# Performance work log

Measured on AMD Instinct MI355X. Metric: run time of the kernel, lower is better.

Reference implementation:

```python
import jax, jax.numpy as jnp
import numpy as np

B, H, S, D = 2, 8, 4096, 64

def setup_inputs() -> dict:
    key = jax.random.key(0)
    kq, kk, kv = jax.random.split(key, 3)
    queries = jax.random.normal(kq, (B, H, S, D), dtype=jnp.float32)
    keys = jax.random.normal(kk, (B, H, S, D), dtype=jnp.float32)
    values = jax.random.normal(kv, (B, H, S, D), dtype=jnp.float32)
    adj = jnp.zeros((1,), dtype=jnp.int32)  # unused by the module, kept for signature fidelity
    return {"queries": queries, "keys": keys, "values": values, "adj": adj}

def reference(queries, keys, values, adj):
    # scores: [B,H,S,S]; note the original divides by a hard-coded 16, not sqrt(d)
    scores = jnp.einsum('bhqd,bhkd->bhqk', queries, keys) / 16.0
    attn = jax.nn.softmax(scores, axis=-1)
    # dropout p=0.0 -> identity in eval/deterministic mode
    h = jnp.einsum('bhqk,bhkd->bhqd', attn, values)  # [B,H,S,D]
    # original uses .view (a reshape, NOT a transpose) to (S, B, H, D)
    return jnp.reshape(h, (S, B, H, D))
```

## Files before the change

kernel.cpp:

```cpp
#include <hip/hip_runtime.h>
#include <hip/hip_bf16.h>
#include <math.h>

#define S_LEN 4096
#define D_DIM 64
#define NBH   16
#define QPRE  0.09016844f

typedef __attribute__((ext_vector_type(8))) short bf16x8;
typedef __attribute__((ext_vector_type(4))) float f32x4;
typedef __attribute__((ext_vector_type(4))) __fp16 f16x4;
typedef __attribute__((ext_vector_type(2))) __fp16 f16x2;

__device__ __forceinline__ unsigned int pkbf(float lo, float hi) {
  unsigned int ua = __float_as_uint(lo) + 0x8000u;
  unsigned int ub = __float_as_uint(hi) + 0x8000u;
  return __builtin_amdgcn_perm(ub, ua, 0x07060302u);
}
__device__ __forceinline__ unsigned int pkhf(float lo, float hi) {
  f16x2 h = __builtin_amdgcn_cvt_pkrtz(lo, hi);
  return *(unsigned int*)&h;
}

__device__ __forceinline__ void dma16(const unsigned short* g, unsigned short* l) {
  __builtin_amdgcn_global_load_lds(
      (const __attribute__((address_space(1))) unsigned int*)g,
      (__attribute__((address_space(3))) unsigned int*)l, 16, 0, 0);
}

__global__ __launch_bounds__(256) void prep(const float* __restrict__ K,
                                            const float* __restrict__ V,
                                            unsigned short* __restrict__ Kbf,
                                            unsigned short* __restrict__ Vt) {
  const int bh = blockIdx.x >> 6;
  const int kt = blockIdx.x & 63;
  const int tid = threadIdx.x;
  __shared__ unsigned short tile[64][72];

  const float* src = V + ((size_t)bh * S_LEN + kt * 64) * D_DIM;
  float4 vf[4];
#pragma unroll
  for (int p = 0; p < 4; ++p) {
    int i = tid + p * 256;
    vf[p] = *(const float4*)&src[(i >> 4) * D_DIM + (i & 15) * 4];
  }
  const float* ks = K + ((size_t)bh * S_LEN + kt * 64) * D_DIM;
  float4 ka[4];
#pragma unroll
  for (int p = 0; p < 2; ++p) {
    int i = tid + p * 256;
    int row = i >> 3, c = (i & 7) * 8;
    ka[2 * p]     = *(const float4*)&ks[row * D_DIM + c];
    ka[2 * p + 1] = *(const float4*)&ks[row * D_DIM + c + 4];
  }

#pragma unroll
  for (int p = 0; p < 4; ++p) {
    int i = tid + p * 256;
    int row = i >> 4, c = (i & 15) * 4;
    int cs = c ^ (((row >> 4) & 3) << 4);
    unsigned long long w = (unsigned long long)pkhf(vf[p].x, vf[p].y) |
                           ((unsigned long long)pkhf(vf[p].z, vf[p].w) << 32);
    *(unsigned long long*)&tile[row][cs] = w;
  }
  __syncthreads();

  unsigned short* kd = Kbf + ((size_t)bh * S_LEN + kt * 64) * D_DIM;
#pragma unroll
  for (int p = 0; p < 2; ++p) {
    int i = tid + p * 256;
    int row = i >> 3, c = (i & 7) * 8;
    uint4 w;
    w.x = pkbf(ka[2 * p].x, ka[2 * p].y);     w.y = pkbf(ka[2 * p].z, ka[2 * p].w);
    w.z = pkbf(ka[2 * p + 1].x, ka[2 * p + 1].y); w.w = pkbf(ka[2 * p + 1].z, ka[2 * p + 1].w);
    *(uint4*)&kd[row * D_DIM + c] = w;
  }

  const int kc = tid & 7;
#pragma unroll
  for (int p = 0; p < 2; ++p) {
    int d = p * 32 + (tid >> 3);
    int col = d ^ (((kc >> 1) & 3) << 4);
    union { unsigned short u[8]; uint4 v; } t;
#pragma unroll
    for (int i = 0; i < 8; ++i) t.u[i] = tile[kc * 8 + i][col];
    *(uint4*)&Vt[((size_t)bh * D_DIM + d) * S_LEN + kt * 64 + kc * 8] = t.v;
  }
}

__global__ __launch_bounds__(256) void fattn(const float* __restrict__ Q,
                                             const unsigned short* __restrict__ Kbf,
                                             const unsigned short* __restrict__ Vt,
                                             float* __restrict__ O) {
  const int bh   = blockIdx.x >> 5;
  const int qb   = blockIdx.x & 31;
  const int tid  = threadIdx.x;
  const int wave = tid >> 6;
  const int lane = tid & 63;
  const int quad = lane >> 4;
  const int l15  = lane & 15;
  const int rho  = l15 & 7;

  __shared__ unsigned short Ksh[2][64][64];
  __shared__ unsigned short Vsh[3][64][64];

  bf16x8 qf[2][2];
#pragma unroll
  for (int qt = 0; qt < 2; ++qt) {
    const int qg = qb * 128 + wave * 32 + qt * 16 + l15;
    const float* qp = Q + ((size_t)bh * S_LEN + qg) * D_DIM + quad * 8;
#pragma unroll
    for (int h = 0; h < 2; ++h) {
      float4 a = *(const float4*)&qp[h * 32];
      float4 b = *(const float4*)&qp[h * 32 + 4];
      union { unsigned int u[4]; bf16x8 v; } f;
      f.u[0] = pkbf(a.x * QPRE, a.y * QPRE);
      f.u[1] = pkbf(a.z * QPRE, a.w * QPRE);
      f.u[2] = pkbf(b.x * QPRE, b.y * QPRE);
      f.u[3] = pkbf(b.z * QPRE, b.w * QPRE);
      qf[qt][h] = f.v;
    }
  }

  f32x4 ot[2][4];
#pragma unroll
  for (int qt = 0; qt < 2; ++qt)
#pragma unroll
    for (int dt = 0; dt < 4; ++dt) ot[qt][dt] = (f32x4){0.f, 0.f, 0.f, 0.f};
  f32x4 otL[2] = {(f32x4){0.f, 0.f, 0.f, 0.f}, (f32x4){0.f, 0.f, 0.f, 0.f}};
  const f16x4 ones = (f16x4){(__fp16)1.0f, (__fp16)1.0f, (__fp16)1.0f, (__fp16)1.0f};

  const unsigned short* Kb = Kbf + (size_t)bh * S_LEN * D_DIM;
  const unsigned short* Vb = Vt + (size_t)bh * D_DIM * S_LEN;

  const int r_lo = wave * 8 + (lane >> 3);
  const int csrc = ((lane & 7) ^ (lane >> 3)) * 8;

  const int ck0 = (quad ^ rho) * 8;
  const int ck1 = ((quad + 4) ^ rho) * 8;
  const int vrow  = l15 * 128 + (quad & 1) * 8;
  const int rho16 = rho << 4;
  const int vq2   = (quad >> 1) << 4;

#define DMAK(T, B) do { const int t_ = (T); \
  dma16(&Kb[(size_t)(t_ * 64 + r_lo) * 64 + csrc],      &Ksh[B][wave * 8][0]); \
  dma16(&Kb[(size_t)(t_ * 64 + r_lo + 32) * 64 + csrc], &Ksh[B][wave * 8 + 32][0]); } while (0)
#define DMAV(T, B) do { const int t_ = (T); \
  dma16(&Vb[(size_t)r_lo * S_LEN + t_ * 64 + csrc],        &Vsh[B][wave * 8][0]); \
  dma16(&Vb[(size_t)(r_lo + 32) * S_LEN + t_ * 64 + csrc], &Vsh[B][wave * 8 + 32][0]); } while (0)

#define SCORES(KB, PD) do { \
  _Pragma("unroll") \
  for (int mt = 0; mt < 4; ++mt) { \
    const int row_ = mt * 16 + l15; \
    bf16x8 kf0 = *(const bf16x8*)&Ksh[KB][row_][ck0]; \
    bf16x8 kf1 = *(const bf16x8*)&Ksh[KB][row_][ck1]; \
    _Pragma("unroll") \
    for (int qt = 0; qt < 2; ++qt) { \
      f32x4 acc = (f32x4){0.f, 0.f, 0.f, 0.f}; \
      acc = __builtin_amdgcn_mfma_f32_16x16x32_bf16(kf0, qf[qt][0], acc, 0, 0, 0); \
      acc = __builtin_amdgcn_mfma_f32_16x16x32_bf16(kf1, qf[qt][1], acc, 0, 0, 0); \
      PD[mt][qt][0] = pkhf(__builtin_amdgcn_exp2f(acc[0]), __builtin_amdgcn_exp2f(acc[1])); \
      PD[mt][qt][1] = pkhf(__builtin_amdgcn_exp2f(acc[2]), __builtin_amdgcn_exp2f(acc[3])); \
    } \
  } } while (0)

#define PVSTEP(VB, PU) do { \
  const char* vbase = (const char*)&Vsh[VB][0][0]; \
  _Pragma("unroll") \
  for (int mt = 0; mt < 4; ++mt) { \
    const int vb_ = vrow + (((mt << 5) + vq2) ^ rho16); \
    union { unsigned int u[2]; f16x4 v; } pb0, pb1; \
    pb0.u[0] = PU[mt][0][0]; pb0.u[1] = PU[mt][0][1]; \
    pb1.u[0] = PU[mt][1][0]; pb1.u[1] = PU[mt][1][1]; \
    otL[0] = __builtin_amdgcn_mfma_f32_16x16x16f16(ones, pb0.v, otL[0], 0, 0, 0); \
    otL[1] = __builtin_amdgcn_mfma_f32_16x16x16f16(ones, pb1.v, otL[1], 0, 0, 0); \
    _Pragma("unroll") \
    for (int dt = 0; dt < 4; ++dt) { \
      f16x4 va = *(const f16x4*)(vbase + vb_ + dt * 2048); \
      ot[0][dt] = __builtin_amdgcn_mfma_f32_16x16x16f16(va, pb0.v, ot[0][dt], 0, 0, 0); \
      ot[1][dt] = __builtin_amdgcn_mfma_f32_16x16x16f16(va, pb1.v, ot[1][dt], 0, 0, 0); \
    } \
  } } while (0)

#define ITER(KT, KBU, KBL, VBU, VBL, PU, PD) do { \
  __syncthreads(); \
  if ((KT) < 62) { DMAK((KT) + 2, KBL); DMAV((KT) + 2, VBL); } \
  SCORES(KBU, PD); \
  PVSTEP(VBU, PU); } while (0)

  unsigned int pA[4][2][2], pB[4][2][2];

  DMAK(0, 0); DMAV(0, 0);
  __syncthreads();
  SCORES(0, pA);
  DMAK(1, 1); DMAV(1, 1);

  for (int b = 0; b < 60; b += 6) {
    ITER(b + 0, 1, 0, 0, 2, pA, pB);
    ITER(b + 1, 0, 1, 1, 0, pB, pA);
    ITER(b + 2, 1, 0, 2, 1, pA, pB);
    ITER(b + 3, 0, 1, 0, 2, pB, pA);
    ITER(b + 4, 1, 0, 1, 0, pA, pB);
    ITER(b + 5, 0, 1, 2, 1, pB, pA);
  }
  ITER(60, 1, 0, 0, 2, pA, pB);
  ITER(61, 0, 1, 1, 0, pB, pA);
  ITER(62, 1, 0, 2, 1, pA, pB);
  PVSTEP(0, pB);

#pragma unroll
  for (int qt = 0; qt < 2; ++qt) {
    float linv = 1.0f / otL[qt][0];
    const int qg = qb * 128 + wave * 32 + qt * 16 + l15;
    float* orow = O + ((size_t)bh * S_LEN + qg) * D_DIM;
#pragma unroll
    for (int dt = 0; dt < 4; ++dt) {
      float4 w;
      w.x = ot[qt][dt][0] * linv;
      w.y = ot[qt][dt][1] * linv;
      w.z = ot[qt][dt][2] * linv;
      w.w = ot[qt][dt][3] * linv;
      *(float4*)&orow[dt * 16 + quad * 4] = w;
    }
  }
#undef DMAK
#undef DMAV
#undef SCORES
#undef PVSTEP
#undef ITER
}

extern "C" void kernel_launch(void* const* d_in, const int* in_sizes, int n_in,
                              void* d_out, int out_size, void* d_ws, size_t ws_size,
                              hipStream_t stream) {
  const float* Q = (const float*)d_in[0];
  const float* K = (const float*)d_in[1];
  const float* V = (const float*)d_in[2];
  unsigned short* Kbf = (unsigned short*)d_ws;
  unsigned short* Vt  = Kbf + (size_t)NBH * S_LEN * D_DIM;
  float* O = (float*)d_out;

  prep<<<NBH * (S_LEN / 64), 256, 0, stream>>>(K, V, Kbf, Vt);
  fattn<<<NBH * (S_LEN / 128), 256, 0, stream>>>(Q, Kbf, Vt, O);
}
```

Measured before the change: 190.1 us.

## Halve queries per block, compute row sums with VALU, shrink V buffering

Each wave now handles 16 query rows instead of 32, so the grid doubles to 1024 blocks and launch bounds ask for 4 blocks per CU. The row-sum MFMA against a ones vector is replaced by accumulating the exp values in registers and reducing across lanes with shuffles. V buffering drops from triple to double, with V prefetched one tile ahead and K two tiles ahead. Block ordering now interleaves heads so neighbouring blocks read different K/V streams. The aim is more occupancy and fewer MFMAs per element, at the cost of K/V tiles being reused across half as many queries per load, which doubles LDS and L2 traffic per query.

```diff
diff --git a/kernel.cpp b/kernel.cpp
--- a/kernel.cpp
+++ b/kernel.cpp
@@ -71,7 +71,7 @@
     int i = tid + p * 256;
     int row = i >> 3, c = (i & 7) * 8;
     uint4 w;
-    w.x = pkbf(ka[2 * p].x, ka[2 * p].y);     w.y = pkbf(ka[2 * p].z, ka[2 * p].w);
+    w.x = pkbf(ka[2 * p].x, ka[2 * p].y);         w.y = pkbf(ka[2 * p].z, ka[2 * p].w);
     w.z = pkbf(ka[2 * p + 1].x, ka[2 * p + 1].y); w.w = pkbf(ka[2 * p + 1].z, ka[2 * p + 1].w);
     *(uint4*)&kd[row * D_DIM + c] = w;
   }
@@ -88,12 +88,12 @@
   }
 }
 
-__global__ __launch_bounds__(256) void fattn(const float* __restrict__ Q,
-                                             const unsigned short* __restrict__ Kbf,
-                                             const unsigned short* __restrict__ Vt,
-                                             float* __restrict__ O) {
-  const int bh   = blockIdx.x >> 5;
-  const int qb   = blockIdx.x & 31;
+__global__ __launch_bounds__(256, 4) void fattn(const float* __restrict__ Q,
+                                                const unsigned short* __restrict__ Kbf,
+                                                const unsigned short* __restrict__ Vt,
+                                                float* __restrict__ O) {
+  const int bh   = blockIdx.x & 15;
+  const int qb   = blockIdx.x >> 4;
   const int tid  = threadIdx.x;
   const int wave = tid >> 6;
   const int lane = tid & 63;
@@ -102,12 +102,11 @@
   const int rho  = l15 & 7;
 
   __shared__ unsigned short Ksh[2][64][64];
-  __shared__ unsigned short Vsh[3][64][64];
-
-  bf16x8 qf[2][2];
-#pragma unroll
-  for (int qt = 0; qt < 2; ++qt) {
-    const int qg = qb * 128 + wave * 32 + qt * 16 + l15;
+  __shared__ unsigned short Vsh[2][64][64];
+
+  bf16x8 qf[2];
+  {
+    const int qg = qb * 64 + wave * 16 + l15;
     const float* qp = Q + ((size_t)bh * S_LEN + qg) * D_DIM + quad * 8;
 #pragma unroll
     for (int h = 0; h < 2; ++h) {
@@ -118,17 +117,14 @@
       f.u[1] = pkbf(a.z * QPRE, a.w * QPRE);
       f.u[2] = pkbf(b.x * QPRE, b.y * QPRE);
       f.u[3] = pkbf(b.z * QPRE, b.w * QPRE);
-      qf[qt][h] = f.v;
+      qf[h] = f.v;
     }
   }
 
-  f32x4 ot[2][4];
-#pragma unroll
-  for (int qt = 0; qt < 2; ++qt)
-#pragma unroll
-    for (int dt = 0; dt < 4; ++dt) ot[qt][dt] = (f32x4){0.f, 0.f, 0.f, 0.f};
-  f32x4 otL[2] = {(f32x4){0.f, 0.f, 0.f, 0.f}, (f32x4){0.f, 0.f, 0.f, 0.f}};
-  const f16x4 ones = (f16x4){(__fp16)1.0f, (__fp16)1.0f, (__fp16)1.0f, (__fp16)1.0f};
+  f32x4 ot[4];
+#pragma unroll
+  for (int dt = 0; dt < 4; ++dt) ot[dt] = (f32x4){0.f, 0.f, 0.f, 0.f};
+  float Lp = 0.f;
 
   const unsigned short* Kb = Kbf + (size_t)bh * S_LEN * D_DIM;
   const unsigned short* Vb = Vt + (size_t)bh * D_DIM * S_LEN;
@@ -155,14 +151,16 @@
     const int row_ = mt * 16 + l15; \
     bf16x8 kf0 = *(const bf16x8*)&Ksh[KB][row_][ck0]; \
     bf16x8 kf1 = *(const bf16x8*)&Ksh[KB][row_][ck1]; \
-    _Pragma("unroll") \
-    for (int qt = 0; qt < 2; ++qt) { \
-      f32x4 acc = (f32x4){0.f, 0.f, 0.f, 0.f}; \
-      acc = __builtin_amdgcn_mfma_f32_16x16x32_bf16(kf0, qf[qt][0], acc, 0, 0, 0); \
-      acc = __builtin_amdgcn_mfma_f32_16x16x32_bf16(kf1, qf[qt][1], acc, 0, 0, 0); \
-      PD[mt][qt][0] = pkhf(__builtin_amdgcn_exp2f(acc[0]), __builtin_amdgcn_exp2f(acc[1])); \
-      PD[mt][qt][1] = pkhf(__builtin_amdgcn_exp2f(acc[2]), __builtin_amdgcn_exp2f(acc[3])); \
-    } \
+    f32x4 acc = (f32x4){0.f, 0.f, 0.f, 0.f}; \
+    acc = __builtin_amdgcn_mfma_f32_16x16x32_bf16(kf0, qf[0], acc, 0, 0, 0); \
+    acc = __builtin_amdgcn_mfma_f32_16x16x32_bf16(kf1, qf[1], acc, 0, 0, 0); \
+    float p0 = __builtin_amdgcn_exp2f(acc[0]); \
+    float p1 = __builtin_amdgcn_exp2f(acc[1]); \
+    float p2 = __builtin_amdgcn_exp2f(acc[2]); \
+    float p3 = __builtin_amdgcn_exp2f(acc[3]); \
+    Lp += (p0 + p1) + (p2 + p3); \
+    PD[mt][0] = pkhf(p0, p1); \
+    PD[mt][1] = pkhf(p2, p3); \
   } } while (0)
 
 #define PVSTEP(VB, PU) do { \
@@ -170,59 +168,51 @@
   _Pragma("unroll") \
   for (int mt = 0; mt < 4; ++mt) { \
     const int vb_ = vrow + (((mt << 5) + vq2) ^ rho16); \
-    union { unsigned int u[2]; f16x4 v; } pb0, pb1; \
-    pb0.u[0] = PU[mt][0][0]; pb0.u[1] = PU[mt][0][1]; \
-    pb1.u[0] = PU[mt][1][0]; pb1.u[1] = PU[mt][1][1]; \
-    otL[0] = __builtin_amdgcn_mfma_f32_16x16x16f16(ones, pb0.v, otL[0], 0, 0, 0); \
-    otL[1] = __builtin_amdgcn_mfma_f32_16x16x16f16(ones, pb1.v, otL[1], 0, 0, 0); \
+    union { unsigned int u[2]; f16x4 v; } pb; \
+    pb.u[0] = PU[mt][0]; pb.u[1] = PU[mt][1]; \
     _Pragma("unroll") \
     for (int dt = 0; dt < 4; ++dt) { \
       f16x4 va = *(const f16x4*)(vbase + vb_ + dt * 2048); \
-      ot[0][dt] = __builtin_amdgcn_mfma_f32_16x16x16f16(va, pb0.v, ot[0][dt], 0, 0, 0); \
-      ot[1][dt] = __builtin_amdgcn_mfma_f32_16x16x16f16(va, pb1.v, ot[1][dt], 0, 0, 0); \
+      ot[dt] = __builtin_amdgcn_mfma_f32_16x16x16f16(va, pb.v, ot[dt], 0, 0, 0); \
     } \
   } } while (0)
 
-#define ITER(KT, KBU, KBL, VBU, VBL, PU, PD) do { \
+#define ITER(KT, KBL, KBU, VBL, VBU, PU, PD) do { \
   __syncthreads(); \
-  if ((KT) < 62) { DMAK((KT) + 2, KBL); DMAV((KT) + 2, VBL); } \
+  if ((KT) < 62) DMAK((KT) + 2, KBL); \
+  DMAV((KT) + 1, VBL); \
   SCORES(KBU, PD); \
   PVSTEP(VBU, PU); } while (0)
 
-  unsigned int pA[4][2][2], pB[4][2][2];
+  unsigned int pA[4][2], pB[4][2];
 
   DMAK(0, 0); DMAV(0, 0);
   __syncthreads();
   SCORES(0, pA);
-  DMAK(1, 1); DMAV(1, 1);
-
-  for (int b = 0; b < 60; b += 6) {
-    ITER(b + 0, 1, 0, 0, 2, pA, pB);
-    ITER(b + 1, 0, 1, 1, 0, pB, pA);
-    ITER(b + 2, 1, 0, 2, 1, pA, pB);
-    ITER(b + 3, 0, 1, 0, 2, pB, pA);
-    ITER(b + 4, 1, 0, 1, 0, pA, pB);
-    ITER(b + 5, 0, 1, 2, 1, pB, pA);
-  }
-  ITER(60, 1, 0, 0, 2, pA, pB);
-  ITER(61, 0, 1, 1, 0, pB, pA);
-  ITER(62, 1, 0, 2, 1, pA, pB);
-  PVSTEP(0, pB);
-
-#pragma unroll
-  for (int qt = 0; qt < 2; ++qt) {
-    float linv = 1.0f / otL[qt][0];
-    const int qg = qb * 128 + wave * 32 + qt * 16 + l15;
-    float* orow = O + ((size_t)bh * S_LEN + qg) * D_DIM;
-#pragma unroll
-    for (int dt = 0; dt < 4; ++dt) {
-      float4 w;
-      w.x = ot[qt][dt][0] * linv;
-      w.y = ot[qt][dt][1] * linv;
-      w.z = ot[qt][dt][2] * linv;
-      w.w = ot[qt][dt][3] * linv;
-      *(float4*)&orow[dt * 16 + quad * 4] = w;
-    }
+  DMAK(1, 1);
+
+  for (int b = 0; b < 62; b += 2) {
+    ITER(b + 0, 0, 1, 1, 0, pA, pB);
+    ITER(b + 1, 1, 0, 0, 1, pB, pA);
+  }
+  ITER(62, 0, 1, 1, 0, pA, pB);
+  __syncthreads();
+  PVSTEP(1, pB);
+
+  float Lt = Lp;
+  Lt += __shfl_xor(Lt, 16);
+  Lt += __shfl_xor(Lt, 32);
+  float linv = 1.0f / Lt;
+  const int qg = qb * 64 + wave * 16 + l15;
+  float* orow = O + ((size_t)bh * S_LEN + qg) * D_DIM;
+#pragma unroll
+  for (int dt = 0; dt < 4; ++dt) {
+    float4 w;
+    w.x = ot[dt][0] * linv;
+    w.y = ot[dt][1] * linv;
+    w.z = ot[dt][2] * linv;
+    w.w = ot[dt][3] * linv;
+    *(float4*)&orow[dt * 16 + quad * 4] = w;
   }
 #undef DMAK
 #undef DMAV
@@ -242,5 +232,5 @@
   float* O = (float*)d_out;
 
   prep<<<NBH * (S_LEN / 64), 256, 0, stream>>>(K, V, Kbf, Vt);
-  fattn<<<NBH * (S_LEN / 128), 256, 0, stream>>>(Q, Kbf, Vt, O);
-}
+  fattn<<<NBH * (S_LEN / 64), 256, 0, stream>>>(Q, Kbf, Vt, O);
+}
```

New measurement: 189.2 us. No clear change (-0.4%).

## Split KV range across two blocks per query tile and reduce partials

Applied to the files above, without the earlier changes.

The attention kernel now splits the key sequence into two halves, each handled by a separate block, which doubles the grid from 512 to 1024 blocks for better CU occupancy. Partial outputs are written as fp16 into the output buffer and partial row sums into workspace, and a new reduce kernel combines and normalises them in place. Row sums are now accumulated with scalar adds instead of extra MFMAs with a ones vector, and the V buffer drops from triple to double buffering. The prep kernel is also restructured to convert K in larger chunks on separate blocks. This adds a third launch and extra global traffic, and the fp16 partials reduce precision. The in-place reduce relies on each block reading its fp16 rows before writing the wider fp32 rows over the same bytes, and __syncthreads only orders threads within a block.

```diff
diff --git a/kernel.cpp b/kernel.cpp
--- a/kernel.cpp
+++ b/kernel.cpp
@@ -5,6 +5,7 @@
 #define S_LEN 4096
 #define D_DIM 64
 #define NBH   16
+#define HKT   32
 #define QPRE  0.09016844f
 
 typedef __attribute__((ext_vector_type(8))) short bf16x8;
@@ -21,7 +22,6 @@
   f16x2 h = __builtin_amdgcn_cvt_pkrtz(lo, hi);
   return *(unsigned int*)&h;
 }
-
 __device__ __forceinline__ void dma16(const unsigned short* g, unsigned short* l) {
   __builtin_amdgcn_global_load_lds(
       (const __attribute__((address_space(1))) unsigned int*)g,
@@ -32,50 +32,38 @@
                                             const float* __restrict__ V,
                                             unsigned short* __restrict__ Kbf,
                                             unsigned short* __restrict__ Vt) {
-  const int bh = blockIdx.x >> 6;
-  const int kt = blockIdx.x & 63;
   const int tid = threadIdx.x;
   __shared__ unsigned short tile[64][72];
-
+  if (blockIdx.x < 256) {
+    const int bh = blockIdx.x >> 4, ch = blockIdx.x & 15;
+    const size_t base = ((size_t)bh * S_LEN + ch * 256) * D_DIM;
+#pragma unroll
+    for (int p = 0; p < 8; ++p) {
+      int i = tid + p * 256;
+      int row = i >> 3, c = (i & 7) * 8;
+      float4 a = *(const float4*)&K[base + row * D_DIM + c];
+      float4 b = *(const float4*)&K[base + row * D_DIM + c + 4];
+      uint4 w;
+      w.x = pkbf(a.x, a.y); w.y = pkbf(a.z, a.w);
+      w.z = pkbf(b.x, b.y); w.w = pkbf(b.z, b.w);
+      *(uint4*)&Kbf[base + row * D_DIM + c] = w;
+    }
+    return;
+  }
+  const int blk = blockIdx.x - 256;
+  const int bh = blk >> 6, kt = blk & 63;
   const float* src = V + ((size_t)bh * S_LEN + kt * 64) * D_DIM;
-  float4 vf[4];
-#pragma unroll
-  for (int p = 0; p < 4; ++p) {
-    int i = tid + p * 256;
-    vf[p] = *(const float4*)&src[(i >> 4) * D_DIM + (i & 15) * 4];
-  }
-  const float* ks = K + ((size_t)bh * S_LEN + kt * 64) * D_DIM;
-  float4 ka[4];
-#pragma unroll
-  for (int p = 0; p < 2; ++p) {
-    int i = tid + p * 256;
-    int row = i >> 3, c = (i & 7) * 8;
-    ka[2 * p]     = *(const float4*)&ks[row * D_DIM + c];
-    ka[2 * p + 1] = *(const float4*)&ks[row * D_DIM + c + 4];
-  }
-
 #pragma unroll
   for (int p = 0; p < 4; ++p) {
     int i = tid + p * 256;
     int row = i >> 4, c = (i & 15) * 4;
+    float4 f = *(const float4*)&src[row * D_DIM + c];
     int cs = c ^ (((row >> 4) & 3) << 4);
-    unsigned long long w = (unsigned long long)pkhf(vf[p].x, vf[p].y) |
-                           ((unsigned long long)pkhf(vf[p].z, vf[p].w) << 32);
+    unsigned long long w = (unsigned long long)pkhf(f.x, f.y) |
+                           ((unsigned long long)pkhf(f.z, f.w) << 32);
     *(unsigned long long*)&tile[row][cs] = w;
   }
   __syncthreads();
-
-  unsigned short* kd = Kbf + ((size_t)bh * S_LEN + kt * 64) * D_DIM;
-#pragma unroll
-  for (int p = 0; p < 2; ++p) {
-    int i = tid + p * 256;
-    int row = i >> 3, c = (i & 7) * 8;
-    uint4 w;
-    w.x = pkbf(ka[2 * p].x, ka[2 * p].y);     w.y = pkbf(ka[2 * p].z, ka[2 * p].w);
-    w.z = pkbf(ka[2 * p + 1].x, ka[2 * p + 1].y); w.w = pkbf(ka[2 * p + 1].z, ka[2 * p + 1].w);
-    *(uint4*)&kd[row * D_DIM + c] = w;
-  }
-
   const int kc = tid & 7;
 #pragma unroll
   for (int p = 0; p < 2; ++p) {
@@ -88,21 +76,24 @@
   }
 }
 
-__global__ __launch_bounds__(256) void fattn(const float* __restrict__ Q,
-                                             const unsigned short* __restrict__ Kbf,
-                                             const unsigned short* __restrict__ Vt,
-                                             float* __restrict__ O) {
-  const int bh   = blockIdx.x >> 5;
-  const int qb   = blockIdx.x & 31;
+__global__ __launch_bounds__(256, 4) void fattn(const float* __restrict__ Q,
+                                                const unsigned short* __restrict__ Kbf,
+                                                const unsigned short* __restrict__ Vt,
+                                                unsigned short* __restrict__ Oh,
+                                                float* __restrict__ Lw) {
+  const int bh   = blockIdx.x & 15;
+  const int qb   = (blockIdx.x >> 4) & 31;
+  const int half = blockIdx.x >> 9;
   const int tid  = threadIdx.x;
   const int wave = tid >> 6;
   const int lane = tid & 63;
   const int quad = lane >> 4;
   const int l15  = lane & 15;
   const int rho  = l15 & 7;
+  const int T0   = half * HKT;
 
   __shared__ unsigned short Ksh[2][64][64];
-  __shared__ unsigned short Vsh[3][64][64];
+  __shared__ unsigned short Vsh[2][64][64];
 
   bf16x8 qf[2][2];
 #pragma unroll
@@ -127,8 +118,7 @@
   for (int qt = 0; qt < 2; ++qt)
 #pragma unroll
     for (int dt = 0; dt < 4; ++dt) ot[qt][dt] = (f32x4){0.f, 0.f, 0.f, 0.f};
-  f32x4 otL[2] = {(f32x4){0.f, 0.f, 0.f, 0.f}, (f32x4){0.f, 0.f, 0.f, 0.f}};
-  const f16x4 ones = (f16x4){(__fp16)1.0f, (__fp16)1.0f, (__fp16)1.0f, (__fp16)1.0f};
+  float Lp[2] = {0.f, 0.f};
 
   const unsigned short* Kb = Kbf + (size_t)bh * S_LEN * D_DIM;
   const unsigned short* Vb = Vt + (size_t)bh * D_DIM * S_LEN;
@@ -160,8 +150,13 @@
       f32x4 acc = (f32x4){0.f, 0.f, 0.f, 0.f}; \
       acc = __builtin_amdgcn_mfma_f32_16x16x32_bf16(kf0, qf[qt][0], acc, 0, 0, 0); \
       acc = __builtin_amdgcn_mfma_f32_16x16x32_bf16(kf1, qf[qt][1], acc, 0, 0, 0); \
-      PD[mt][qt][0] = pkhf(__builtin_amdgcn_exp2f(acc[0]), __builtin_amdgcn_exp2f(acc[1])); \
-      PD[mt][qt][1] = pkhf(__builtin_amdgcn_exp2f(acc[2]), __builtin_amdgcn_exp2f(acc[3])); \
+      float p0 = __builtin_amdgcn_exp2f(acc[0]); \
+      float p1 = __builtin_amdgcn_exp2f(acc[1]); \
+      float p2 = __builtin_amdgcn_exp2f(acc[2]); \
+      float p3 = __builtin_amdgcn_exp2f(acc[3]); \
+      Lp[qt] += (p0 + p1) + (p2 + p3); \
+      PD[mt][qt][0] = pkhf(p0, p1); \
+      PD[mt][qt][1] = pkhf(p2, p3); \
     } \
   } } while (0)
 
@@ -173,8 +168,6 @@
     union { unsigned int u[2]; f16x4 v; } pb0, pb1; \
     pb0.u[0] = PU[mt][0][0]; pb0.u[1] = PU[mt][0][1]; \
     pb1.u[0] = PU[mt][1][0]; pb1.u[1] = PU[mt][1][1]; \
-    otL[0] = __builtin_amdgcn_mfma_f32_16x16x16f16(ones, pb0.v, otL[0], 0, 0, 0); \
-    otL[1] = __builtin_amdgcn_mfma_f32_16x16x16f16(ones, pb1.v, otL[1], 0, 0, 0); \
     _Pragma("unroll") \
     for (int dt = 0; dt < 4; ++dt) { \
       f16x4 va = *(const f16x4*)(vbase + vb_ + dt * 2048); \
@@ -183,45 +176,41 @@
     } \
   } } while (0)
 
-#define ITER(KT, KBU, KBL, VBU, VBL, PU, PD) do { \
+#define ITER(I, KBL, KBU, VBL, VBU, PU, PD) do { \
   __syncthreads(); \
-  if ((KT) < 62) { DMAK((KT) + 2, KBL); DMAV((KT) + 2, VBL); } \
+  if ((I) < HKT - 2) DMAK(T0 + (I) + 2, KBL); \
+  DMAV(T0 + (I) + 1, VBL); \
   SCORES(KBU, PD); \
   PVSTEP(VBU, PU); } while (0)
 
   unsigned int pA[4][2][2], pB[4][2][2];
 
-  DMAK(0, 0); DMAV(0, 0);
+  DMAK(T0, 0); DMAV(T0, 0);
   __syncthreads();
   SCORES(0, pA);
-  DMAK(1, 1); DMAV(1, 1);
-
-  for (int b = 0; b < 60; b += 6) {
-    ITER(b + 0, 1, 0, 0, 2, pA, pB);
-    ITER(b + 1, 0, 1, 1, 0, pB, pA);
-    ITER(b + 2, 1, 0, 2, 1, pA, pB);
-    ITER(b + 3, 0, 1, 0, 2, pB, pA);
-    ITER(b + 4, 1, 0, 1, 0, pA, pB);
-    ITER(b + 5, 0, 1, 2, 1, pB, pA);
-  }
-  ITER(60, 1, 0, 0, 2, pA, pB);
-  ITER(61, 0, 1, 1, 0, pB, pA);
-  ITER(62, 1, 0, 2, 1, pA, pB);
-  PVSTEP(0, pB);
+  DMAK(T0 + 1, 1);
+
+  for (int b = 0; b < HKT - 2; b += 2) {
+    ITER(b + 0, 0, 1, 1, 0, pA, pB);
+    ITER(b + 1, 1, 0, 0, 1, pB, pA);
+  }
+  ITER(HKT - 2, 0, 1, 1, 0, pA, pB);
+  __syncthreads();
+  PVSTEP(1, pB);
 
 #pragma unroll
   for (int qt = 0; qt < 2; ++qt) {
-    float linv = 1.0f / otL[qt][0];
-    const int qg = qb * 128 + wave * 32 + qt * 16 + l15;
-    float* orow = O + ((size_t)bh * S_LEN + qg) * D_DIM;
+    float Lt = Lp[qt];
+    Lt += __shfl_xor(Lt, 16);
+    Lt += __shfl_xor(Lt, 32);
+    const size_t grow = (size_t)bh * S_LEN + qb * 128 + wave * 32 + qt * 16 + l15;
+    if (quad == 0) Lw[grow * 2 + half] = Lt;
 #pragma unroll
     for (int dt = 0; dt < 4; ++dt) {
-      float4 w;
-      w.x = ot[qt][dt][0] * linv;
-      w.y = ot[qt][dt][1] * linv;
-      w.z = ot[qt][dt][2] * linv;
-      w.w = ot[qt][dt][3] * linv;
-      *(float4*)&orow[dt * 16 + quad * 4] = w;
+      uint2 w;
+      w.x = pkhf(ot[qt][dt][0], ot[qt][dt][1]);
+      w.y = pkhf(ot[qt][dt][2], ot[qt][dt][3]);
+      *(uint2*)&Oh[grow * 128 + half * 64 + dt * 16 + quad * 4] = w;
     }
   }
 #undef DMAK
@@ -229,6 +218,25 @@
 #undef SCORES
 #undef PVSTEP
 #undef ITER
+}
+
+__global__ __launch_bounds__(256) void reduce(unsigned short* Oh, const float* __restrict__ Lw) {
+  const int tid = threadIdx.x;
+  const size_t r = (size_t)blockIdx.x * 32 + (tid >> 3);
+  const int d0 = (tid & 7) * 8;
+  union { uint4 v; __fp16 h[8]; } a, b;
+  a.v = *(const uint4*)&Oh[r * 128 + d0];
+  b.v = *(const uint4*)&Oh[r * 128 + 64 + d0];
+  const float linv = 1.0f / (Lw[r * 2] + Lw[r * 2 + 1]);
+  float o[8];
+#pragma unroll
+  for (int j = 0; j < 8; ++j) o[j] = ((float)a.h[j] + (float)b.h[j]) * linv;
+  __syncthreads();
+  float* Of = (float*)Oh;
+  float4 w0 = {o[0], o[1], o[2], o[3]};
+  float4 w1 = {o[4], o[5], o[6], o[7]};
+  *(float4*)&Of[r * 64 + d0]     = w0;
+  *(float4*)&Of[r * 64 + d0 + 4] = w1;
 }
 
 extern "C" void kernel_launch(void* const* d_in, const int* in_sizes, int n_in,
@@ -239,8 +247,10 @@
   const float* V = (const float*)d_in[2];
   unsigned short* Kbf = (unsigned short*)d_ws;
   unsigned short* Vt  = Kbf + (size_t)NBH * S_LEN * D_DIM;
-  float* O = (float*)d_out;
-
-  prep<<<NBH * (S_LEN / 64), 256, 0, stream>>>(K, V, Kbf, Vt);
-  fattn<<<NBH * (S_LEN / 128), 256, 0, stream>>>(Q, Kbf, Vt, O);
-}
+  float* Lw = (float*)(Vt + (size_t)NBH * S_LEN * D_DIM);
+  unsigned short* Oh = (unsigned short*)d_out;
+
+  prep<<<1280, 256, 0, stream>>>(K, V, Kbf, Vt);
+  fattn<<<NBH * 32 * 2, 256, 0, stream>>>(Q, Kbf, Vt, Oh, Lw);
+  reduce<<<(NBH * S_LEN) / 32, 256, 0, stream>>>(Oh, Lw);
+}
```

Result: no change. 187.9 us (-1.1%).
